# Kernel tuning notes

Measured on AMD Instinct MI355X. Metric: run time of the kernel, lower is better.

Reference implementation:

```python
import jax, jax.numpy as jnp
import numpy as np

EPS = 1e-6

def _feature_map(x):
    # elu(x) + 1 == where(x > 0, x + 1, exp(x))
    return jnp.where(x > 0, x + 1.0, jnp.exp(x))

def setup_inputs() -> dict:
    key = jax.random.key(0)
    kq, kk, kv = jax.random.split(key, 3)
    B, H, L, D = 4, 16, 8192, 64
    q = jax.random.normal(kq, (B, H, L, D), dtype=jnp.float32)
    k = jax.random.normal(kk, (B, H, L, D), dtype=jnp.float32)
    v = jax.random.normal(kv, (B, H, L, D), dtype=jnp.float32)
    attention_mask = jnp.ones((B, L), dtype=jnp.float32)
    return {"q": q, "k": k, "v": v, "attention_mask": attention_mask}

def reference(q, k, v, attention_mask):
    # feature-mapped queries/keys (compute_scores)
    q = _feature_map(q)
    k = _feature_map(k)
    # mask keys/values: mask shape [B,L] -> [B,1,L,1]
    mask = attention_mask[:, None, :, None]
    k = k * mask
    v = v * mask
    # causal branch: cumulative sums along sequence dim
    k_cumsum = jnp.cumsum(k, axis=2)            # [B,H,L,D]
    kv_cumsum = jnp.cumsum(k * v, axis=2)       # [B,H,L,D]
    z = jnp.einsum('bhld,bhld->bhl', q, k_cumsum) + EPS
    z = z * attention_mask[:, None, :]
    output = q * kv_cumsum                       # einsum 'bhld,bhld->bhld' is elementwise
    output = output / z[..., None]
    return output
```

## Files before the change

kernel.cpp:

```cpp
#include <hip/hip_runtime.h>
#include <cstdint>

#define EPS 1e-6f

constexpr int Bsz = 4, Hn = 16, Lseq = 8192, Dd = 64;
constexpr int BH = Bsz * Hn;
constexpr int CHUNK = 128;
constexpr int CPB = Lseq / CHUNK;
constexpr int NCHUNKS = BH * CPB;
constexpr int WPB = 4;
constexpr int R = 4;
constexpr int SUB = 4 * R;

__device__ __forceinline__ float phi(float x) {
    return x > 0.0f ? x + 1.0f : __expf(x);
}

__global__ __launch_bounds__(256) void partials_kernel(
    const float* __restrict__ k, const float* __restrict__ v,
    const float* __restrict__ mask,
    float* __restrict__ pk, float* __restrict__ pkv)
{
    const int wave = blockIdx.x * WPB + (threadIdx.x >> 6);
    const int lane = threadIdx.x & 63;
    const int rg = lane >> 4;
    const int dg = lane & 15;
    const int bh = wave / CPB;
    const int c  = wave % CPB;
    const int b  = bh / Hn;
    const int l0 = c * CHUNK;

    float4 ak  = make_float4(0.f, 0.f, 0.f, 0.f);
    float4 akv = make_float4(0.f, 0.f, 0.f, 0.f);

    for (int i = 0; i < CHUNK; i += 4) {
        const int l = l0 + i + rg;
        const size_t off = ((size_t)bh * Lseq + l) * Dd + dg * 4;
        const float4 k4 = *(const float4*)(k + off);
        const float4 v4 = *(const float4*)(v + off);
        const float m = mask[(size_t)b * Lseq + l];
        float t;
        t = phi(k4.x) * m; ak.x += t; akv.x += t * (v4.x * m);
        t = phi(k4.y) * m; ak.y += t; akv.y += t * (v4.y * m);
        t = phi(k4.z) * m; ak.z += t; akv.z += t * (v4.z * m);
        t = phi(k4.w) * m; ak.w += t; akv.w += t * (v4.w * m);
    }

    #pragma unroll
    for (int off = 16; off <= 32; off <<= 1) {
        ak.x  += __shfl_xor(ak.x,  off, 64);
        ak.y  += __shfl_xor(ak.y,  off, 64);
        ak.z  += __shfl_xor(ak.z,  off, 64);
        ak.w  += __shfl_xor(ak.w,  off, 64);
        akv.x += __shfl_xor(akv.x, off, 64);
        akv.y += __shfl_xor(akv.y, off, 64);
        akv.z += __shfl_xor(akv.z, off, 64);
        akv.w += __shfl_xor(akv.w, off, 64);
    }

    if (rg == 0) {
        const size_t o = (size_t)wave * Dd + dg * 4;
        *(float4*)(pk  + o) = ak;
        *(float4*)(pkv + o) = akv;
    }
}

__global__ __launch_bounds__(256) void scan_kernel(
    float* __restrict__ pk, float* __restrict__ pkv)
{
    const int w    = blockIdx.x * 4 + (threadIdx.x >> 6);
    const int lane = threadIdx.x & 63;
    const int bh   = w >> 6;
    const int d    = w & 63;
    const size_t o = ((size_t)(bh * CPB + lane)) * Dd + d;
    const float tk  = pk[o];
    const float tkv = pkv[o];
    float ik = tk, ikv = tkv;
    #pragma unroll
    for (int off = 1; off <= 32; off <<= 1) {
        const float t1 = __shfl_up(ik,  off, 64);
        const float t2 = __shfl_up(ikv, off, 64);
        if (lane >= off) { ik += t1; ikv += t2; }
    }
    pk[o]  = ik  - tk;
    pkv[o] = ikv - tkv;
}

__global__ __launch_bounds__(256) void final_kernel(
    const float* __restrict__ q, const float* __restrict__ k,
    const float* __restrict__ v, const float* __restrict__ mask,
    const float* __restrict__ pk, const float* __restrict__ pkv,
    float* __restrict__ out)
{
    const int wave = blockIdx.x * WPB + (threadIdx.x >> 6);
    const int lane = threadIdx.x & 63;
    const int rg = lane >> 4;
    const int dg = lane & 15;
    const int bh = wave / CPB;
    const int c  = wave % CPB;
    const int b  = bh / Hn;
    const int l0 = c * CHUNK;

    const size_t po = (size_t)wave * Dd + dg * 4;
    float4 Sk  = *(const float4*)(pk  + po);
    float4 Skv = *(const float4*)(pkv + po);

    for (int s = 0; s < CHUNK / SUB; ++s) {
        const int lbase = l0 + s * SUB + rg * R;

        float4 pa[R], pakv[R];
        float  ms[R];
        float4 ra   = make_float4(0.f, 0.f, 0.f, 0.f);
        float4 rakv = make_float4(0.f, 0.f, 0.f, 0.f);

        #pragma unroll
        for (int j = 0; j < R; ++j) {
            const int l = lbase + j;
            const size_t off = ((size_t)bh * Lseq + l) * Dd + dg * 4;
            const float4 k4 = *(const float4*)(k + off);
            const float4 v4 = *(const float4*)(v + off);
            const float m = mask[(size_t)b * Lseq + l];
            ms[j] = m;
            float t;
            t = phi(k4.x) * m; ra.x += t; rakv.x += t * (v4.x * m);
            t = phi(k4.y) * m; ra.y += t; rakv.y += t * (v4.y * m);
            t = phi(k4.z) * m; ra.z += t; rakv.z += t * (v4.z * m);
            t = phi(k4.w) * m; ra.w += t; rakv.w += t * (v4.w * m);
            pa[j]   = ra;
            pakv[j] = rakv;
        }

        float4 ia = ra, iakv = rakv;
        float t;
        t = __shfl_up(ia.x,   16, 64); if (rg >= 1) ia.x   += t;
        t = __shfl_up(ia.y,   16, 64); if (rg >= 1) ia.y   += t;
        t = __shfl_up(ia.z,   16, 64); if (rg >= 1) ia.z   += t;
        t = __shfl_up(ia.w,   16, 64); if (rg >= 1) ia.w   += t;
        t = __shfl_up(iakv.x, 16, 64); if (rg >= 1) iakv.x += t;
        t = __shfl_up(iakv.y, 16, 64); if (rg >= 1) iakv.y += t;
        t = __shfl_up(iakv.z, 16, 64); if (rg >= 1) iakv.z += t;
        t = __shfl_up(iakv.w, 16, 64); if (rg >= 1) iakv.w += t;
        t = __shfl_up(ia.x,   32, 64); if (rg >= 2) ia.x   += t;
        t = __shfl_up(ia.y,   32, 64); if (rg >= 2) ia.y   += t;
        t = __shfl_up(ia.z,   32, 64); if (rg >= 2) ia.z   += t;
        t = __shfl_up(ia.w,   32, 64); if (rg >= 2) ia.w   += t;
        t = __shfl_up(iakv.x, 32, 64); if (rg >= 2) iakv.x += t;
        t = __shfl_up(iakv.y, 32, 64); if (rg >= 2) iakv.y += t;
        t = __shfl_up(iakv.z, 32, 64); if (rg >= 2) iakv.z += t;
        t = __shfl_up(iakv.w, 32, 64); if (rg >= 2) iakv.w += t;

        const float4 ofk = make_float4(Sk.x + ia.x - ra.x, Sk.y + ia.y - ra.y,
                                       Sk.z + ia.z - ra.z, Sk.w + ia.w - ra.w);
        const float4 ofkv = make_float4(Skv.x + iakv.x - rakv.x, Skv.y + iakv.y - rakv.y,
                                        Skv.z + iakv.z - rakv.z, Skv.w + iakv.w - rakv.w);

        Sk.x  += __shfl(ia.x,   48 + dg, 64);
        Sk.y  += __shfl(ia.y,   48 + dg, 64);
        Sk.z  += __shfl(ia.z,   48 + dg, 64);
        Sk.w  += __shfl(ia.w,   48 + dg, 64);
        Skv.x += __shfl(iakv.x, 48 + dg, 64);
        Skv.y += __shfl(iakv.y, 48 + dg, 64);
        Skv.z += __shfl(iakv.z, 48 + dg, 64);
        Skv.w += __shfl(iakv.w, 48 + dg, 64);

        #pragma unroll
        for (int j = 0; j < R; ++j) {
            const int l = lbase + j;
            const size_t off = ((size_t)bh * Lseq + l) * Dd + dg * 4;
            const float4 q4 = *(const float4*)(q + off);
            const float m = ms[j];

            float4 fq;
            fq.x = phi(q4.x); fq.y = phi(q4.y); fq.z = phi(q4.z); fq.w = phi(q4.w);

            const float4 ik  = make_float4(ofk.x  + pa[j].x,   ofk.y  + pa[j].y,
                                           ofk.z  + pa[j].z,   ofk.w  + pa[j].w);
            const float4 ikv = make_float4(ofkv.x + pakv[j].x, ofkv.y + pakv[j].y,
                                           ofkv.z + pakv[j].z, ofkv.w + pakv[j].w);

            float p = fq.x * ik.x + fq.y * ik.y + fq.z * ik.z + fq.w * ik.w;
            p += __shfl_xor(p, 1, 64);
            p += __shfl_xor(p, 2, 64);
            p += __shfl_xor(p, 4, 64);
            p += __shfl_xor(p, 8, 64);
            const float z = (p + EPS) * m;
            const float inv = 1.0f / z;

            float4 o4;
            o4.x = fq.x * ikv.x * inv;
            o4.y = fq.y * ikv.y * inv;
            o4.z = fq.z * ikv.z * inv;
            o4.w = fq.w * ikv.w * inv;
            *(float4*)(out + off) = o4;
        }
    }
}

extern "C" void kernel_launch(void* const* d_in, const int* in_sizes, int n_in,
                              void* d_out, int out_size, void* d_ws, size_t ws_size,
                              hipStream_t stream) {
    const float* q    = (const float*)d_in[0];
    const float* k    = (const float*)d_in[1];
    const float* v    = (const float*)d_in[2];
    const float* mask = (const float*)d_in[3];
    float* out = (float*)d_out;

    float* pk  = (float*)d_ws;
    float* pkv = pk + (size_t)NCHUNKS * Dd;

    partials_kernel<<<NCHUNKS / WPB, 256, 0, stream>>>(k, v, mask, pk, pkv);
    scan_kernel<<<(BH * Dd) / 4, 256, 0, stream>>>(pk, pkv);
    final_kernel<<<NCHUNKS / WPB, 256, 0, stream>>>(q, k, v, mask, pk, pkv, out);
}
```

Measured before the change: 449.1 us.

## Halve chunk size, batch loads ahead of compute, use nontemporal output stores

```diff
diff --git a/kernel.cpp b/kernel.cpp
--- a/kernel.cpp
+++ b/kernel.cpp
@@ -5,12 +5,14 @@
 
 constexpr int Bsz = 4, Hn = 16, Lseq = 8192, Dd = 64;
 constexpr int BH = Bsz * Hn;
-constexpr int CHUNK = 128;
+constexpr int CHUNK = 64;
 constexpr int CPB = Lseq / CHUNK;
 constexpr int NCHUNKS = BH * CPB;
 constexpr int WPB = 4;
 constexpr int R = 4;
 constexpr int SUB = 4 * R;
+
+typedef float vfloat4 __attribute__((ext_vector_type(4)));
 
 __device__ __forceinline__ float phi(float x) {
     return x > 0.0f ? x + 1.0f : __expf(x);
@@ -33,17 +35,25 @@
     float4 ak  = make_float4(0.f, 0.f, 0.f, 0.f);
     float4 akv = make_float4(0.f, 0.f, 0.f, 0.f);
 
-    for (int i = 0; i < CHUNK; i += 4) {
-        const int l = l0 + i + rg;
-        const size_t off = ((size_t)bh * Lseq + l) * Dd + dg * 4;
-        const float4 k4 = *(const float4*)(k + off);
-        const float4 v4 = *(const float4*)(v + off);
-        const float m = mask[(size_t)b * Lseq + l];
-        float t;
-        t = phi(k4.x) * m; ak.x += t; akv.x += t * (v4.x * m);
-        t = phi(k4.y) * m; ak.y += t; akv.y += t * (v4.y * m);
-        t = phi(k4.z) * m; ak.z += t; akv.z += t * (v4.z * m);
-        t = phi(k4.w) * m; ak.w += t; akv.w += t * (v4.w * m);
+    for (int i = 0; i < CHUNK; i += 16) {
+        float4 k4[4], v4[4];
+        float  m[4];
+        #pragma unroll
+        for (int u = 0; u < 4; ++u) {
+            const int l = l0 + i + 4 * u + rg;
+            const size_t off = ((size_t)bh * Lseq + l) * Dd + dg * 4;
+            k4[u] = *(const float4*)(k + off);
+            v4[u] = *(const float4*)(v + off);
+            m[u]  = mask[(size_t)b * Lseq + l];
+        }
+        #pragma unroll
+        for (int u = 0; u < 4; ++u) {
+            float t;
+            t = phi(k4[u].x) * m[u]; ak.x += t; akv.x += t * (v4[u].x * m[u]);
+            t = phi(k4[u].y) * m[u]; ak.y += t; akv.y += t * (v4[u].y * m[u]);
+            t = phi(k4[u].z) * m[u]; ak.z += t; akv.z += t * (v4[u].z * m[u]);
+            t = phi(k4[u].w) * m[u]; ak.w += t; akv.w += t * (v4[u].w * m[u]);
+        }
     }
 
     #pragma unroll
@@ -72,18 +82,26 @@
     const int lane = threadIdx.x & 63;
     const int bh   = w >> 6;
     const int d    = w & 63;
-    const size_t o = ((size_t)(bh * CPB + lane)) * Dd + d;
-    const float tk  = pk[o];
-    const float tkv = pkv[o];
-    float ik = tk, ikv = tkv;
+    const int c0   = lane * 2;
+    const size_t o0 = ((size_t)(bh * CPB + c0)) * Dd + d;
+    const size_t o1 = o0 + Dd;
+
+    const float tk0  = pk[o0],  tk1  = pk[o1];
+    const float tkv0 = pkv[o0], tkv1 = pkv[o1];
+    const float sk  = tk0 + tk1;
+    const float skv = tkv0 + tkv1;
+
+    float ik = sk, ikv = skv;
     #pragma unroll
     for (int off = 1; off <= 32; off <<= 1) {
         const float t1 = __shfl_up(ik,  off, 64);
         const float t2 = __shfl_up(ikv, off, 64);
         if (lane >= off) { ik += t1; ikv += t2; }
     }
-    pk[o]  = ik  - tk;
-    pkv[o] = ikv - tkv;
+    const float ek  = ik  - sk;
+    const float ekv = ikv - skv;
+    pk[o0]  = ek;          pkv[o0] = ekv;
+    pk[o1]  = ek + tk0;    pkv[o1] = ekv + tkv0;
 }
 
 __global__ __launch_bounds__(256) void final_kernel(
@@ -108,24 +126,30 @@
     for (int s = 0; s < CHUNK / SUB; ++s) {
         const int lbase = l0 + s * SUB + rg * R;
 
-        float4 pa[R], pakv[R];
+        float4 k4[R], v4[R], q4[R];
         float  ms[R];
-        float4 ra   = make_float4(0.f, 0.f, 0.f, 0.f);
-        float4 rakv = make_float4(0.f, 0.f, 0.f, 0.f);
-
         #pragma unroll
         for (int j = 0; j < R; ++j) {
             const int l = lbase + j;
             const size_t off = ((size_t)bh * Lseq + l) * Dd + dg * 4;
-            const float4 k4 = *(const float4*)(k + off);
-            const float4 v4 = *(const float4*)(v + off);
-            const float m = mask[(size_t)b * Lseq + l];
-            ms[j] = m;
+            k4[j] = *(const float4*)(k + off);
+            v4[j] = *(const float4*)(v + off);
+            q4[j] = *(const float4*)(q + off);
+            ms[j] = mask[(size_t)b * Lseq + l];
+        }
+
+        float4 pa[R], pakv[R];
+        float4 ra   = make_float4(0.f, 0.f, 0.f, 0.f);
+        float4 rakv = make_float4(0.f, 0.f, 0.f, 0.f);
+
+        #pragma unroll
+        for (int j = 0; j < R; ++j) {
+            const float m = ms[j];
             float t;
-            t = phi(k4.x) * m; ra.x += t; rakv.x += t * (v4.x * m);
-            t = phi(k4.y) * m; ra.y += t; rakv.y += t * (v4.y * m);
-            t = phi(k4.z) * m; ra.z += t; rakv.z += t * (v4.z * m);
-            t = phi(k4.w) * m; ra.w += t; rakv.w += t * (v4.w * m);
+            t = phi(k4[j].x) * m; ra.x += t; rakv.x += t * (v4[j].x * m);
+            t = phi(k4[j].y) * m; ra.y += t; rakv.y += t * (v4[j].y * m);
+            t = phi(k4[j].z) * m; ra.z += t; rakv.z += t * (v4[j].z * m);
+            t = phi(k4[j].w) * m; ra.w += t; rakv.w += t * (v4[j].w * m);
             pa[j]   = ra;
             pakv[j] = rakv;
         }
@@ -167,11 +191,11 @@
         for (int j = 0; j < R; ++j) {
             const int l = lbase + j;
             const size_t off = ((size_t)bh * Lseq + l) * Dd + dg * 4;
-            const float4 q4 = *(const float4*)(q + off);
             const float m = ms[j];
 
             float4 fq;
-            fq.x = phi(q4.x); fq.y = phi(q4.y); fq.z = phi(q4.z); fq.w = phi(q4.w);
+            fq.x = phi(q4[j].x); fq.y = phi(q4[j].y);
+            fq.z = phi(q4[j].z); fq.w = phi(q4[j].w);
 
             const float4 ik  = make_float4(ofk.x  + pa[j].x,   ofk.y  + pa[j].y,
                                            ofk.z  + pa[j].z,   ofk.w  + pa[j].w);
@@ -186,12 +210,12 @@
             const float z = (p + EPS) * m;
             const float inv = 1.0f / z;
 
-            float4 o4;
+            vfloat4 o4;
             o4.x = fq.x * ikv.x * inv;
             o4.y = fq.y * ikv.y * inv;
             o4.z = fq.z * ikv.z * inv;
             o4.w = fq.w * ikv.w * inv;
-            *(float4*)(out + off) = o4;
+            __builtin_nontemporal_store(o4, (vfloat4*)(out + off));
         }
     }
 }
```

New measurement: 453.5 us. Within noise of the previous version (+1.0%).
